# Kernel optimization log

Measured on AMD Instinct MI355X. Metric: run time of the kernel, lower is better.

Reference implementation:

```python
import jax, jax.numpy as jnp
import numpy as np

B = 131072      # batch
N = 128         # taxonomy nodes (level-order)
G = 32          # sibling groups (disjoint masks covering all nodes)
ALPHA = 0.5
EPS = 1e-10


def setup_inputs() -> dict:
    key = jax.random.key(0)
    k1, k2 = jax.random.split(key)
    logits = jax.random.normal(k1, (B, N), dtype=jnp.float32)
    # hierarchical multi-hot targets (ones along taxonomy paths); sparse 0/1 floats
    true = (jax.random.uniform(k2, (B, N)) < 0.05).astype(jnp.float32)
    # sibling groups: 32 disjoint groups of 4 siblings each
    group_ids = jnp.repeat(jnp.arange(G, dtype=jnp.int32), N // G)
    # node depths in the tree (balanced-binary-tree style depths)
    depths = jnp.asarray(np.floor(np.log2(np.arange(N) + 1)), dtype=jnp.float32)
    return {"logits": logits, "true": true, "depths": depths, "group_ids": group_ids}


def reference(logits, true, depths, group_ids):
    # class weights: N_samples / (N_nodes * (counts + eps))
    n_samples = logits.shape[0]
    class_weights = n_samples / (N * (jnp.sum(true, axis=0) + EPS))  # [N]

    # The torch loop applies a masked softmax per disjoint sibling mask; since
    # masks are disjoint and cover all nodes, this is one segment-softmax over
    # sibling groups: softmax_i = exp(x_i) / (sum_{j in group(i)} exp(x_j) + eps)
    onehot = jax.nn.one_hot(group_ids, G, dtype=logits.dtype)       # [N, G]
    exps = jnp.exp(logits)                                          # [B, N]
    group_sums = exps @ onehot                                      # [B, G]
    denom = group_sums @ onehot.T + EPS                             # [B, N]
    logp = jnp.log(exps / denom)                                    # [B, N]

    lam = jnp.exp(-ALPHA * depths)                                  # [N]
    v1 = jnp.sum(class_weights * (logp * lam) * true, axis=1)       # [B]
    return -jnp.mean(v1)
```

## Files before the change

### kernel.cpp

```cpp
#include <hip/hip_runtime.h>


#define B_TOTAL 131072
#define N_NODES 128
#define ALPHA   0.5f
#define EPS     1e-10f

constexpr int BLOCKS         = 2048;
constexpr int THREADS        = 256;
constexpr int ROWS_PER_ITER  = THREADS / 32;
constexpr int ROWS_PER_BLOCK = B_TOTAL / BLOCKS;
constexpr int ITERS          = ROWS_PER_BLOCK / ROWS_PER_ITER;
constexpr int REPLICAS       = 32;

__global__ __launch_bounds__(THREADS, 8) void whxe_pass1(
    const float* __restrict__ logits,
    const float* __restrict__ truev,
    const float* __restrict__ depths,
    float* __restrict__ ws)
{
    const int t    = threadIdx.x;
    const int cg   = t & 31;
    const int rsub = t >> 5;
    const int c0   = cg << 2;

    float lam[4];
#pragma unroll
    for (int i = 0; i < 4; ++i) lam[i] = __expf(-ALPHA * depths[c0 + i]);

    float colS[4] = {0.f, 0.f, 0.f, 0.f};
    float cnt [4] = {0.f, 0.f, 0.f, 0.f};

    const size_t base0 = (size_t)(blockIdx.x * ROWS_PER_BLOCK + rsub) * N_NODES + c0;
    const float* lp = logits + base0;
    const float* tp = truev  + base0;
    constexpr size_t STRIDE = (size_t)ROWS_PER_ITER * N_NODES;

    float4 x  = *reinterpret_cast<const float4*>(lp);
    float4 tv = *reinterpret_cast<const float4*>(tp);
#pragma unroll
    for (int it = 0; it < ITERS; ++it) {
        float4 xn, tvn;
        if (it + 1 < ITERS) {
            xn  = *reinterpret_cast<const float4*>(lp + (size_t)(it + 1) * STRIDE);
            tvn = *reinterpret_cast<const float4*>(tp + (size_t)(it + 1) * STRIDE);
        }
        const float e0 = __expf(x.x), e1 = __expf(x.y),
                    e2 = __expf(x.z), e3 = __expf(x.w);
        const float ld = __logf(e0 + e1 + e2 + e3 + EPS);
        colS[0] += lam[0] * (x.x - ld) * tv.x;  cnt[0] += tv.x;
        colS[1] += lam[1] * (x.y - ld) * tv.y;  cnt[1] += tv.y;
        colS[2] += lam[2] * (x.z - ld) * tv.z;  cnt[2] += tv.z;
        colS[3] += lam[3] * (x.w - ld) * tv.w;  cnt[3] += tv.w;
        x = xn; tv = tvn;
    }

    __shared__ float lds[8][THREADS];
#pragma unroll
    for (int i = 0; i < 4; ++i) {
        lds[i][t]     = colS[i];
        lds[4 + i][t] = cnt[i];
    }
    __syncthreads();

    const int q   = t >> 7;
    const int c   = t & 127;
    const int acc = q * 4 + (c & 3);
    const int cgr = c >> 2;
    float s = 0.f;
#pragma unroll
    for (int r = 0; r < 8; ++r) s += lds[acc][r * 32 + cgr];

    const int rep = blockIdx.x & (REPLICAS - 1);
    atomicAdd(&ws[rep * 256 + q * 128 + c], s);
}

__global__ __launch_bounds__(256) void whxe_pass2(
    const float* __restrict__ ws, float* __restrict__ out)
{
    const int t = threadIdx.x;
    float s = 0.f;
#pragma unroll
    for (int r = 0; r < REPLICAS; ++r) s += ws[r * 256 + t];

    __shared__ float red[256];
    red[t] = s;
    __syncthreads();

    float v = 0.f;
    if (t < 128) {
        const float w = (float)B_TOTAL / ((float)N_NODES * (red[128 + t] + EPS));
        v = w * red[t];
    }
    __syncthreads();
    red[t] = v;
    __syncthreads();

    if (t < 64) {
        float r2 = red[t] + red[t + 64] + ((t < 128) ? red[t + 128] + red[t + 192] : 0.f);
#pragma unroll
        for (int off = 32; off; off >>= 1) r2 += __shfl_xor(r2, off);
        if (t == 0) out[0] = -r2 / (float)B_TOTAL;
    }
}

extern "C" void kernel_launch(void* const* d_in, const int* in_sizes, int n_in,
                              void* d_out, int out_size, void* d_ws, size_t ws_size,
                              hipStream_t stream) {
    const float* logits = (const float*)d_in[0];
    const float* truev  = (const float*)d_in[1];
    const float* depths = (const float*)d_in[2];
    float* ws = (float*)d_ws;

    hipMemsetAsync(ws, 0, REPLICAS * 256 * sizeof(float), stream);
    whxe_pass1<<<BLOCKS, THREADS, 0, stream>>>(logits, truev, depths, ws);
    whxe_pass2<<<1, 256, 0, stream>>>(ws, (float*)d_out);
}
```

Measured before the change: 32.26 us.

## Stream input tiles through triple-buffered LDS with async global_load_lds

The main pass stops using register-prefetched float4 loads. Each wave now issues direct global-to-LDS loads (`__builtin_amdgcn_global_load_lds`) into a three-slot ring of 8-row tiles, keeps two tiles in flight, and paces consumption with explicit `s_waitcnt vmcnt` counts. The aim is deeper memory-level parallelism on a bandwidth-bound streaming reduction, at the cost of 24 KB of LDS per block, removal of the minimum-occupancy launch bound, and hand-managed wait counts. The finalize kernel also folds the class-weighted sum into one 64-thread loop, dropping two block barriers.

```diff
diff --git a/kernel.cpp b/kernel.cpp
--- a/kernel.cpp
+++ b/kernel.cpp
@@ -8,43 +8,64 @@
 
 constexpr int BLOCKS         = 2048;
 constexpr int THREADS        = 256;
-constexpr int ROWS_PER_ITER  = THREADS / 32;
 constexpr int ROWS_PER_BLOCK = B_TOTAL / BLOCKS;
-constexpr int ITERS          = ROWS_PER_BLOCK / ROWS_PER_ITER;
+constexpr int TILE_ROWS      = 8;
+constexpr int NT             = ROWS_PER_BLOCK / TILE_ROWS;
+constexpr int SLOT_FLOATS    = 2 * TILE_ROWS * N_NODES;
+constexpr int SLOTS          = 3;
 constexpr int REPLICAS       = 32;
 
-__global__ __launch_bounds__(THREADS, 8) void whxe_pass1(
+typedef const __attribute__((address_space(1))) void* gas_t;
+typedef __attribute__((address_space(3)))       void* las_t;
+
+__global__ __launch_bounds__(THREADS) void whxe_pass1(
     const float* __restrict__ logits,
     const float* __restrict__ truev,
     const float* __restrict__ depths,
     float* __restrict__ ws)
 {
-    const int t    = threadIdx.x;
-    const int cg   = t & 31;
-    const int rsub = t >> 5;
-    const int c0   = cg << 2;
+    __shared__ float lds[SLOTS * SLOT_FLOATS];
+
+    const int t  = threadIdx.x;
+    const int wv = t >> 6;
+    const int cg = t & 31;
+    const int c0 = cg << 2;
 
     float lam[4];
 #pragma unroll
     for (int i = 0; i < 4; ++i) lam[i] = __expf(-ALPHA * depths[c0 + i]);
 
+    const size_t blk = (size_t)blockIdx.x * ROWS_PER_BLOCK * N_NODES;
+    const float* gl = logits + blk + t * 4;
+    const float* gt = truev  + blk + t * 4;
+
+#define STAGE(k)                                                              \
+    do {                                                                      \
+        float* lb = &lds[((k) % SLOTS) * SLOT_FLOATS + wv * 256];             \
+        __builtin_amdgcn_global_load_lds((gas_t)(gl + (size_t)(k) * 1024),    \
+                                         (las_t)lb,           16, 0, 0);      \
+        __builtin_amdgcn_global_load_lds((gas_t)(gt + (size_t)(k) * 1024),    \
+                                         (las_t)(lb + 1024),  16, 0, 0);      \
+    } while (0)
+
+    STAGE(0);
+    STAGE(1);
+
     float colS[4] = {0.f, 0.f, 0.f, 0.f};
     float cnt [4] = {0.f, 0.f, 0.f, 0.f};
 
-    const size_t base0 = (size_t)(blockIdx.x * ROWS_PER_BLOCK + rsub) * N_NODES + c0;
-    const float* lp = logits + base0;
-    const float* tp = truev  + base0;
-    constexpr size_t STRIDE = (size_t)ROWS_PER_ITER * N_NODES;
+#pragma unroll
+    for (int k = 0; k < NT; ++k) {
+        if (k + 2 < NT) STAGE(k + 2);
+        if      (k < NT - 2) asm volatile("s_waitcnt vmcnt(4)" ::: "memory");
+        else if (k == NT - 2) asm volatile("s_waitcnt vmcnt(2)" ::: "memory");
+        else                  asm volatile("s_waitcnt vmcnt(0)" ::: "memory");
+        __builtin_amdgcn_sched_barrier(0);
 
-    float4 x  = *reinterpret_cast<const float4*>(lp);
-    float4 tv = *reinterpret_cast<const float4*>(tp);
-#pragma unroll
-    for (int it = 0; it < ITERS; ++it) {
-        float4 xn, tvn;
-        if (it + 1 < ITERS) {
-            xn  = *reinterpret_cast<const float4*>(lp + (size_t)(it + 1) * STRIDE);
-            tvn = *reinterpret_cast<const float4*>(tp + (size_t)(it + 1) * STRIDE);
-        }
+        const int s4 = (k % SLOTS) * SLOT_FLOATS + t * 4;
+        const float4 x  = *reinterpret_cast<const float4*>(&lds[s4]);
+        const float4 tv = *reinterpret_cast<const float4*>(&lds[s4 + 1024]);
+
         const float e0 = __expf(x.x), e1 = __expf(x.y),
                     e2 = __expf(x.z), e3 = __expf(x.w);
         const float ld = __logf(e0 + e1 + e2 + e3 + EPS);
@@ -52,14 +73,14 @@
         colS[1] += lam[1] * (x.y - ld) * tv.y;  cnt[1] += tv.y;
         colS[2] += lam[2] * (x.z - ld) * tv.z;  cnt[2] += tv.z;
         colS[3] += lam[3] * (x.w - ld) * tv.w;  cnt[3] += tv.w;
-        x = xn; tv = tvn;
     }
+#undef STAGE
 
-    __shared__ float lds[8][THREADS];
+    __syncthreads();
 #pragma unroll
     for (int i = 0; i < 4; ++i) {
-        lds[i][t]     = colS[i];
-        lds[4 + i][t] = cnt[i];
+        lds[i * 256 + t]       = colS[i];
+        lds[(4 + i) * 256 + t] = cnt[i];
     }
     __syncthreads();
 
@@ -69,7 +90,7 @@
     const int cgr = c >> 2;
     float s = 0.f;
 #pragma unroll
-    for (int r = 0; r < 8; ++r) s += lds[acc][r * 32 + cgr];
+    for (int r = 0; r < 8; ++r) s += lds[acc * 256 + r * 32 + cgr];
 
     const int rep = blockIdx.x & (REPLICAS - 1);
     atomicAdd(&ws[rep * 256 + q * 128 + c], s);
@@ -87,20 +108,16 @@
     red[t] = s;
     __syncthreads();
 
-    float v = 0.f;
-    if (t < 128) {
-        const float w = (float)B_TOTAL / ((float)N_NODES * (red[128 + t] + EPS));
-        v = w * red[t];
-    }
-    __syncthreads();
-    red[t] = v;
-    __syncthreads();
-
     if (t < 64) {
-        float r2 = red[t] + red[t + 64] + ((t < 128) ? red[t + 128] + red[t + 192] : 0.f);
+        float v = 0.f;
 #pragma unroll
-        for (int off = 32; off; off >>= 1) r2 += __shfl_xor(r2, off);
-        if (t == 0) out[0] = -r2 / (float)B_TOTAL;
+        for (int cc = t; cc < 128; cc += 64) {
+            const float w = (float)B_TOTAL / ((float)N_NODES * (red[128 + cc] + EPS));
+            v += w * red[cc];
+        }
+#pragma unroll
+        for (int off = 32; off; off >>= 1) v += __shfl_xor(v, off);
+        if (t == 0) out[0] = -v / (float)B_TOTAL;
     }
 }
 
```

Result: slower. 34.01 us (+5.4%).
